# Optimization experiments

Hardware: AMD Instinct MI355X
Metric: run time of the kernel (lower is better)

The kernel has to match this reference:

```python
import jax, jax.numpy as jnp
import numpy as np

GROUP_SIZES = [5, 5, 5, 5, 5, 5, 4]  # 7 concept groups, sum = 34
LN_EPS = 1e-5


def setup_inputs() -> dict:
    key = jax.random.key(0)
    ks = jax.random.split(key, 12)
    B, N, D, K, P, C, NC, H = 256, 196, 768, 7, 512, 34, 7, 3072
    img_feat_map = jax.random.normal(ks[0], (B, N, D), dtype=jnp.float32)
    # torch: Embedding weight uniform in [-1/K, 1/K]
    vq_codebook = (jax.random.uniform(ks[1], (K, D), dtype=jnp.float32) * 2.0 - 1.0) / K
    agg_codebook = jax.random.normal(ks[2], (K, D), dtype=jnp.float32)
    W1 = jax.random.normal(ks[3], (D, H), dtype=jnp.float32) * 0.02
    b1 = jnp.zeros((H,), dtype=jnp.float32)
    W2 = jax.random.normal(ks[4], (H, D), dtype=jnp.float32) * 0.02
    b2 = jnp.zeros((D,), dtype=jnp.float32)
    ln_gamma = jnp.ones((D,), dtype=jnp.float32)
    ln_beta = jnp.zeros((D,), dtype=jnp.float32)
    W_proj = jax.random.normal(ks[5], (D, P), dtype=jnp.float32) * 0.02
    concept_emb = jax.random.normal(ks[6], (C, P), dtype=jnp.float32)
    concept_emb = concept_emb / jnp.linalg.norm(concept_emb, axis=-1, keepdims=True)
    cls_W = jax.random.normal(ks[7], (C, NC), dtype=jnp.float32) * 0.02
    cls_b = jnp.zeros((NC,), dtype=jnp.float32)
    logit_scale = jnp.float32(100.0)  # detached CLIP logit scale
    return {
        "img_feat_map": img_feat_map, "vq_codebook": vq_codebook,
        "agg_codebook": agg_codebook, "W1": W1, "b1": b1, "W2": W2, "b2": b2,
        "ln_gamma": ln_gamma, "ln_beta": ln_beta, "W_proj": W_proj,
        "concept_emb": concept_emb, "cls_W": cls_W, "cls_b": cls_b,
        "logit_scale": logit_scale,
    }


def _pairwise_sq_dists(x, cb):
    # x: [B, N, D], cb: [K, D] -> [B, N, K]
    x_sq = jnp.sum(x * x, axis=-1, keepdims=True)           # [B, N, 1]
    cb_sq = jnp.sum(cb * cb, axis=-1)                        # [K]
    dot = jnp.einsum("bnd,kd->bnk", x, cb)                  # [B, N, K]
    return x_sq + cb_sq - 2.0 * dot


def _avg_effective_rank(x, threshold=0.99):
    # x: [B, N, D]; per-sample SVD, rank = #{cumsum(S)/sum(S) <= thr}
    S = jnp.linalg.svd(jax.lax.stop_gradient(x), compute_uv=False)  # [B, min(N,D)]
    energy = jnp.cumsum(S, axis=-1) / jnp.sum(S, axis=-1, keepdims=True)
    ranks = jnp.sum(energy <= threshold, axis=-1)
    return jnp.mean(ranks.astype(jnp.float32))


def reference(img_feat_map, vq_codebook, agg_codebook, W1, b1, W2, b2,
              ln_gamma, ln_beta, W_proj, concept_emb, cls_W, cls_b, logit_scale):
    x = img_feat_map  # [B, N, D]

    avg_rank = _avg_effective_rank(x)

    # --- VectorQuantizeAggregator: soft assignment to 7 codes ---
    d_agg = _pairwise_sq_dists(x, agg_codebook)              # [B, N, K]
    soft = jax.nn.softmax(-d_agg, axis=-1)                   # [B, N, K]
    agg = jnp.einsum("bnk,bnd->bkd", soft, x)               # [B, K, D]

    # --- VectorQuantizer: hard argmin + gather (one-hot @ codebook) ---
    d_vq = _pairwise_sq_dists(x, vq_codebook)                # [B, N, K]
    idx = jnp.argmin(d_vq, axis=-1)                          # [B, N] int
    quantized = vq_codebook[idx]                             # [B, N, D] gather == onehot @ cb
    sg = jax.lax.stop_gradient
    codebook_loss = jnp.mean((quantized - sg(x)) ** 2)
    commitment_loss = jnp.mean((sg(quantized) - x) ** 2)
    vq_loss = codebook_loss + 1.0 * commitment_loss

    # --- bridge: FFN -> LayerNorm -> proj -> L2 normalize ---
    h = jax.nn.gelu(agg @ W1 + b1, approximate=False) @ W2 + b2  # [B, K, D]
    mu = jnp.mean(h, axis=-1, keepdims=True)
    var = jnp.mean((h - mu) ** 2, axis=-1, keepdims=True)
    hn = (h - mu) * jax.lax.rsqrt(var + LN_EPS) * ln_gamma + ln_beta
    tok = hn @ W_proj                                        # [B, K, 512]
    tok = tok / jnp.linalg.norm(tok, axis=-1, keepdims=True)

    # --- per-group concept logits: token g vs its concept slice ---
    logits_list = []
    start = 0
    for g, sz in enumerate(GROUP_SIZES):
        ce = concept_emb[start:start + sz]                   # [sz, 512]
        logits_list.append(logit_scale * (tok[:, g, :] @ ce.T))  # [B, sz]
        start += sz
    image_logits = jnp.concatenate(logits_list, axis=-1)     # [B, 34]

    cls_logits = image_logits @ cls_W + cls_b                # [B, 7]
    return (cls_logits, image_logits, vq_loss, avg_rank)
```

## Files before the change

kernel.cpp:

```cpp
#include <hip/hip_runtime.h>
#include <hip/hip_bf16.h>
#include <math.h>

using hbf = __hip_bfloat16;
typedef __bf16 bf16x8 __attribute__((ext_vector_type(8)));
typedef float f32x4 __attribute__((ext_vector_type(4)));

__device__ inline float r16d(float v){
  int x;
  x = __builtin_bit_cast(int, v);
  v += __builtin_bit_cast(float, __builtin_amdgcn_mov_dpp(x, 0x121, 0xf, 0xf, true));
  x = __builtin_bit_cast(int, v);
  v += __builtin_bit_cast(float, __builtin_amdgcn_mov_dpp(x, 0x122, 0xf, 0xf, true));
  x = __builtin_bit_cast(int, v);
  v += __builtin_bit_cast(float, __builtin_amdgcn_mov_dpp(x, 0x124, 0xf, 0xf, true));
  x = __builtin_bit_cast(int, v);
  v += __builtin_bit_cast(float, __builtin_amdgcn_mov_dpp(x, 0x128, 0xf, 0xf, true));
  return v;
}
__device__ inline void r16d4(float& a, float& b, float& c, float& d){
#define R16STAGE(ctl) { \
  int xa=__builtin_bit_cast(int,a), xb=__builtin_bit_cast(int,b); \
  int xc=__builtin_bit_cast(int,c), xd=__builtin_bit_cast(int,d); \
  a += __builtin_bit_cast(float, __builtin_amdgcn_mov_dpp(xa, ctl, 0xf, 0xf, true)); \
  b += __builtin_bit_cast(float, __builtin_amdgcn_mov_dpp(xb, ctl, 0xf, 0xf, true)); \
  c += __builtin_bit_cast(float, __builtin_amdgcn_mov_dpp(xc, ctl, 0xf, 0xf, true)); \
  d += __builtin_bit_cast(float, __builtin_amdgcn_mov_dpp(xd, ctl, 0xf, 0xf, true)); }
  R16STAGE(0x121) R16STAGE(0x122) R16STAGE(0x124) R16STAGE(0x128)
#undef R16STAGE
}
__device__ inline float wred(float v){
  v = r16d(v);
  v += __shfl_xor(v, 16);
  v += __shfl_xor(v, 32);
  return v;
}
__device__ inline float fast_rcp(float x){
  float r; asm("v_rcp_f32 %0, %1" : "=v"(r) : "v"(x)); return r;
}
__device__ inline float d4(const float4& a, const float4& b){
  return a.x*b.x + a.y*b.y + a.z*b.z + a.w*b.w;
}

__global__ void k_init(float* scal){
  if (threadIdx.x < 2) scal[threadIdx.x] = 0.f;
}

__global__ __launch_bounds__(512) void k_dist(const float* __restrict__ x,
    const float* __restrict__ vqcb, const float* __restrict__ agcb,
    hbf* __restrict__ aggbf, float* __restrict__ scal){
  __shared__ float cA[5376];
  __shared__ float cV[5376];
  __shared__ float sqA[7], sqV[7];
  const int tid = threadIdx.x, lane = tid & 63, wave = tid >> 6;
  const int b = blockIdx.x;
  for (int i = tid; i < 5376; i += 512){ cA[i] = agcb[i]; cV[i] = vqcb[i]; }
  __syncthreads();
  {
    int grp = tid >> 4, l16 = tid & 15;
    if (grp < 14){
      const float* s = (grp < 7) ? &cA[grp*768] : &cV[(grp-7)*768];
      float acc = 0.f;
      for (int j = l16; j < 768; j += 16) acc += s[j]*s[j];
      acc = r16d(acc);
      if (l16 == 0){ if (grp < 7) sqA[grp] = acc; else sqV[grp-7] = acc; }
    }
  }
  __syncthreads();
  float sqAr[7], sqVr[7];
#pragma unroll
  for (int k = 0; k < 7; ++k){ sqAr[k] = sqA[k]; sqVr[k] = sqV[k]; }

  float4 aR[7][3];
#pragma unroll
  for (int k = 0; k < 7; ++k)
#pragma unroll
    for (int c = 0; c < 3; ++c) aR[k][c] = make_float4(0.f,0.f,0.f,0.f);
  float loss = 0.f;

  const float* xb = x + (size_t)b*196*768;
  float4 cx0, cx1, cx2, nx0, nx1, nx2;
  { const float* p = xb + (size_t)wave*768 + (lane<<2);
    cx0 = *(const float4*)(p); cx1 = *(const float4*)(p+256); cx2 = *(const float4*)(p+512); }
  for (int it = 0; it < 25; ++it){
    const int n = it*8 + wave;
    const int nn = n + 8;
    if (nn < 196){
      const float* p = xb + (size_t)nn*768 + (lane<<2);
      nx0 = *(const float4*)(p); nx1 = *(const float4*)(p+256); nx2 = *(const float4*)(p+512);
    }
    if (n < 196){
      float xsq = d4(cx0,cx0)+d4(cx1,cx1)+d4(cx2,cx2);
      float dA[7], dV[7];
#pragma unroll
      for (int k = 0; k < 7; ++k){
        const float4* pa = (const float4*)&cA[k*768];
        const float4* pv = (const float4*)&cV[k*768];
        float4 a0 = pa[lane], a1 = pa[64+lane], a2 = pa[128+lane];
        float4 q0 = pv[lane], q1 = pv[64+lane], q2 = pv[128+lane];
        dA[k] = d4(cx0,a0)+d4(cx1,a1)+d4(cx2,a2);
        dV[k] = d4(cx0,q0)+d4(cx1,q1)+d4(cx2,q2);
      }
      xsq = wred(xsq);
#pragma unroll
      for (int k = 0; k < 7; ++k){ dA[k] = wred(dA[k]); dV[k] = wred(dV[k]); }
      float lg[7], mx = -1e30f;
#pragma unroll
      for (int k = 0; k < 7; ++k){ lg[k] = 2.f*dA[k] - sqAr[k]; mx = fmaxf(mx, lg[k]); }
      float pr[7], ssum = 0.f;
#pragma unroll
      for (int k = 0; k < 7; ++k){ pr[k] = expf(lg[k]-mx); ssum += pr[k]; }
      const float inv = 1.f/ssum;
      float mn = 1e30f;
#pragma unroll
      for (int k = 0; k < 7; ++k) mn = fminf(mn, sqVr[k] - 2.f*dV[k]);
      loss += xsq + mn;
#pragma unroll
      for (int k = 0; k < 7; ++k){
        const float w = pr[k]*inv;
        aR[k][0].x += w*cx0.x; aR[k][0].y += w*cx0.y; aR[k][0].z += w*cx0.z; aR[k][0].w += w*cx0.w;
        aR[k][1].x += w*cx1.x; aR[k][1].y += w*cx1.y; aR[k][1].z += w*cx1.z; aR[k][1].w += w*cx1.w;
        aR[k][2].x += w*cx2.x; aR[k][2].y += w*cx2.y; aR[k][2].z += w*cx2.z; aR[k][2].w += w*cx2.w;
      }
    }
    cx0 = nx0; cx1 = nx1; cx2 = nx2;
  }
  __syncthreads();
  for (int i = tid; i < 5376; i += 512) cA[i] = 0.f;
  __syncthreads();
  for (int w = 0; w < 8; ++w){
    if (wave == w){
#pragma unroll
      for (int k = 0; k < 7; ++k)
#pragma unroll
        for (int c = 0; c < 3; ++c){
          float* p = &cA[k*768 + c*256 + (lane<<2)];
          p[0] += aR[k][c].x; p[1] += aR[k][c].y; p[2] += aR[k][c].z; p[3] += aR[k][c].w;
        }
    }
    __syncthreads();
  }
  for (int i = tid; i < 5376; i += 512) aggbf[(size_t)b*5376 + i] = __float2bfloat16(cA[i]);
  if (lane == 0) atomicAdd(&scal[0], loss);
}

__global__ __launch_bounds__(512) void k_gram(const float* __restrict__ x, float* __restrict__ G){
  __shared__ hbf Xs[208*104];
  const int tid = threadIdx.x, lane = tid & 63, wave = tid >> 6;
  const int b = blockIdx.x;
  const int l15 = lane & 15;
  const int fr0 = wave, fr1 = wave + 8;
  const bool f1 = (fr1 < 13);
  f32x4 acc0[13] = {};
  f32x4 acc1[13] = {};
  const float* xb = x + (size_t)b*196*768;
  for (int kc = 0; kc < 8; ++kc){
    __syncthreads();
    for (int u = tid; u < 4992; u += 512){
      const int r = u / 24, c4 = u - r*24;
      ushort4 val;
      if (r < 196){
        float4 f = *(const float4*)(xb + (size_t)r*768 + kc*96 + c4*4);
        hbf t0 = __float2bfloat16(f.x), t1 = __float2bfloat16(f.y);
        hbf t2 = __float2bfloat16(f.z), t3 = __float2bfloat16(f.w);
        val.x = *(const unsigned short*)&t0; val.y = *(const unsigned short*)&t1;
        val.z = *(const unsigned short*)&t2; val.w = *(const unsigned short*)&t3;
      } else { val.x = 0; val.y = 0; val.z = 0; val.w = 0; }
      *(ushort4*)&Xs[r*104 + c4*4] = val;
    }
    __syncthreads();
#pragma unroll
    for (int kk = 0; kk < 3; ++kk){
      const int ko = kk*32 + (lane>>4)*8;
      bf16x8 a0 = *(const bf16x8*)&Xs[(fr0*16 + l15)*104 + ko];
      bf16x8 a1 = f1 ? *(const bf16x8*)&Xs[(fr1*16 + l15)*104 + ko] : a0;
#pragma unroll
      for (int fc = 0; fc < 13; ++fc){
        bf16x8 bb = *(const bf16x8*)&Xs[(fc*16 + l15)*104 + ko];
        acc0[fc] = __builtin_amdgcn_mfma_f32_16x16x32_bf16(a0, bb, acc0[fc], 0, 0, 0);
        if (f1) acc1[fc] = __builtin_amdgcn_mfma_f32_16x16x32_bf16(a1, bb, acc1[fc], 0, 0, 0);
      }
    }
  }
  const size_t gb = (size_t)b*38416;
  const int cr = (lane>>4)*4;
#pragma unroll
  for (int fc = 0; fc < 13; ++fc){
    const int gc = fc*16 + l15;
    if (gc < 196){
#pragma unroll
      for (int r = 0; r < 4; ++r){
        const int gr = fr0*16 + cr + r;
        if (gr < 196) G[gb + (size_t)gr*196 + gc] = acc0[fc][r];
      }
      if (f1){
#pragma unroll
        for (int r = 0; r < 4; ++r){
          const int gr = fr1*16 + cr + r;
          if (gr < 196) G[gb + (size_t)gr*196 + gc] = acc1[fc][r];
        }
      }
    }
  }
}

#define ESTR 200
#define FOLD4(vv4) { vv4.x = (oc==0)? v0 : vv4.x; vv4.y = (oc==1)? v0 : vv4.y; \
                     vv4.z = (oc==2)? v0 : vv4.z; vv4.w = (oc==3)? v0 : vv4.w; }
#define VHOIST(colc, out) { \
  const int col_ = (colc) + jc4; \
  const float4 xv_ = *(const float4*)(rowk + col_); \
  float4 vp_; \
  if (col_ > base){ vp_ = xv_; } \
  else if (col_ + 3 <= base){ vp_ = make_float4(0.f,0.f,0.f,0.f); } \
  else { vp_.x = 0.f; \
         vp_.y = (col_+1 > base) ? xv_.y : 0.f; \
         vp_.z = (col_+2 > base) ? xv_.z : 0.f; \
         vp_.w = xv_.w; } \
  out = vp_; sig += vp_.x*vp_.x + vp_.y*vp_.y + vp_.z*vp_.z + vp_.w*vp_.w; }

__global__ __launch_bounds__(1024) void k_eigen(const float* __restrict__ G, float* __restrict__ scal){
  extern __shared__ float S[];
  float* A   = S;
  float* ww  = S + 39200;
  float* dd  = S + 39456;
  float* ee  = S + 39656;
  float* e2  = S + 39856;
  float* red2= S + 40056;
  const int n = 196;
  const int tid = threadIdx.x, lane = tid & 63, wave = tid >> 6;
  const int grp = lane >> 4, c16 = lane & 15;
  const int jc4 = c16 << 2;
  const int rbase = (wave << 2) + grp;
  const int b = blockIdx.x;
  {
    const float4* Gv = (const float4*)(G + (size_t)b*38416);
    for (int u = tid; u < 9604; u += 1024){
      const int r = u / 49, c4 = u - r*49;
      *(float4*)(A + (size_t)r*ESTR + (c4<<2)) = Gv[u];
    }
    for (int r = tid; r < 196; r += 1024)
      *(float4*)(A + (size_t)r*ESTR + 196) = make_float4(0.f,0.f,0.f,0.f);
    if (tid < 256) ww[tid] = 0.f;
  }
  __syncthreads();
  for (int k = 0; k <= 130; ++k){
    const int base = k + 1, m = n - 1 - k;
    const float* rowk = &A[(size_t)k*ESTR];
    const float x0 = rowk[base];
    if (tid == 0) ww[k] = 0.f;
    float4 v4_0, v4_1, v4_2, v4_3;
    float sig = 0.f;
    VHOIST(0,   v4_0)
    VHOIST(64,  v4_1)
    VHOIST(128, v4_2)
    {
      const int col_ = 192 + jc4;
      const float4 xv_ = *(const float4*)(rowk + col_);
      if (c16 == 0){ v4_3 = xv_; sig += xv_.x*xv_.x + xv_.y*xv_.y + xv_.z*xv_.z + xv_.w*xv_.w; }
      else v4_3 = make_float4(0.f,0.f,0.f,0.f);
    }
    sig = r16d(sig);
    float tau = 0.f, v0 = 0.f, alpha = x0;
    if (sig > 1e-20f){
      const float mu = sqrtf(x0*x0 + sig);
      alpha = (x0 > 0.f) ? -mu : mu;
      v0 = x0 - alpha;
      tau = 2.f/(sig + v0*v0);
    }
    if (tid == 0) ee[k] = alpha;
    if (c16 == ((base >> 2) & 15)){
      const int oc = base & 3;
      const int op = base >> 6;
      if (op == 0){ FOLD4(v4_0) } else if (op == 1){ FOLD4(v4_1) } else { FOLD4(v4_2) }
    }
    const int p0 = base >> 6;
    const int i0 = rbase, i1 = 64 + rbase, i2 = 128 + rbase, i3 = 192 + rbase;
    float vr_0=0.f, vr_1=0.f, vr_2=0.f, vr_3=0.f;
    float wr_0=0.f, wr_1=0.f, wr_2=0.f, wr_3=0.f;
    if (tau != 0.f){
      float a0c=0.f, a1c=0.f, a2c=0.f, a3c=0.f;
      {
        const float* Ar = &A[(size_t)(base+i0)*ESTR];
        if (0 >= p0) a0c += d4(*(const float4*)(Ar + jc4),       v4_0);
        if (1 >= p0) a0c += d4(*(const float4*)(Ar + 64 + jc4),  v4_1);
        if (2 >= p0) a0c += d4(*(const float4*)(Ar + 128 + jc4), v4_2);
        a0c += d4(*(const float4*)(Ar + 192 + jc4), v4_3);
      }
      if (i1 < m){
        const float* Ar = &A[(size_t)(base+i1)*ESTR];
        if (0 >= p0) a1c += d4(*(const float4*)(Ar + jc4),       v4_0);
        if (1 >= p0) a1c += d4(*(const float4*)(Ar + 64 + jc4),  v4_1);
        if (2 >= p0) a1c += d4(*(const float4*)(Ar + 128 + jc4), v4_2);
        a1c += d4(*(const float4*)(Ar + 192 + jc4), v4_3);
      }
      if (i2 < m){
        const float* Ar = &A[(size_t)(base+i2)*ESTR];
        if (0 >= p0) a2c += d4(*(const float4*)(Ar + jc4),       v4_0);
        if (1 >= p0) a2c += d4(*(const float4*)(Ar + 64 + jc4),  v4_1);
        if (2 >= p0) a2c += d4(*(const float4*)(Ar + 128 + jc4), v4_2);
        a2c += d4(*(const float4*)(Ar + 192 + jc4), v4_3);
      }
      if (i3 < m){
        const float* Ar = &A[(size_t)(base+i3)*ESTR];
        if (0 >= p0) a3c += d4(*(const float4*)(Ar + jc4),       v4_0);
        if (1 >= p0) a3c += d4(*(const float4*)(Ar + 64 + jc4),  v4_1);
        if (2 >= p0) a3c += d4(*(const float4*)(Ar + 128 + jc4), v4_2);
        a3c += d4(*(const float4*)(Ar + 192 + jc4), v4_3);
      }
      r16d4(a0c, a1c, a2c, a3c);
      float cpart = 0.f;
      {
        wr_0 = tau*a0c;
        vr_0 = (i0 == 0) ? v0 : rowk[base+i0];
        cpart += vr_0*wr_0;
        if (c16 == 0) ww[base+i0] = wr_0;
      }
      if (i1 < m){
        wr_1 = tau*a1c; vr_1 = rowk[base+i1];
        cpart += vr_1*wr_1;
        if (c16 == 0) ww[base+i1] = wr_1;
      }
      if (i2 < m){
        wr_2 = tau*a2c; vr_2 = rowk[base+i2];
        cpart += vr_2*wr_2;
        if (c16 == 0) ww[base+i2] = wr_2;
      }
      if (i3 < m){
        wr_3 = tau*a3c; vr_3 = rowk[base+i3];
        cpart += vr_3*wr_3;
        if (c16 == 0) ww[base+i3] = wr_3;
      }
      cpart += __shfl_xor(cpart, 16);
      cpart += __shfl_xor(cpart, 32);
      if (lane == 0) red2[wave] = cpart;
    }
    __syncthreads();
    if (tau != 0.f){
      const float4* r2 = (const float4*)red2;
      const float4 q0 = r2[0], q1 = r2[1], q2 = r2[2], q3 = r2[3];
      const float vtw = (q0.x+q0.y+q0.z+q0.w) + (q1.x+q1.y+q1.z+q1.w)
                      + (q2.x+q2.y+q2.z+q2.w) + (q3.x+q3.y+q3.z+q3.w);
      const float c2 = 0.5f*tau*vtw;
      float4 w4_0, w4_1, w4_2, w4_3;
      { const float4 t4 = *(const float4*)(ww + jc4);
        w4_0.x = t4.x - c2*v4_0.x; w4_0.y = t4.y - c2*v4_0.y; w4_0.z = t4.z - c2*v4_0.z; w4_0.w = t4.w - c2*v4_0.w; }
      { const float4 t4 = *(const float4*)(ww + 64 + jc4);
        w4_1.x = t4.x - c2*v4_1.x; w4_1.y = t4.y - c2*v4_1.y; w4_1.z = t4.z - c2*v4_1.z; w4_1.w = t4.w - c2*v4_1.w; }
      { const float4 t4 = *(const float4*)(ww + 128 + jc4);
        w4_2.x = t4.x - c2*v4_2.x; w4_2.y = t4.y - c2*v4_2.y; w4_2.z = t4.z - c2*v4_2.z; w4_2.w = t4.w - c2*v4_2.w; }
      { const float4 t4 = *(const float4*)(ww + 192 + jc4);
        w4_3.x = t4.x - c2*v4_3.x; w4_3.y = t4.y - c2*v4_3.y; w4_3.z = t4.z - c2*v4_3.z; w4_3.w = t4.w - c2*v4_3.w; }
#define UP_T(IV, VRV, WRV) { \
      if (IV < m){ \
        const float vi = VRV; \
        const float wi = WRV - c2*vi; \
        float* Ar = &A[(size_t)(base+IV)*ESTR]; \
        if (0 >= p0){ float4 a = *(const float4*)(Ar + jc4); \
          a.x -= vi*w4_0.x + wi*v4_0.x; a.y -= vi*w4_0.y + wi*v4_0.y; \
          a.z -= vi*w4_0.z + wi*v4_0.z; a.w -= vi*w4_0.w + wi*v4_0.w; \
          *(float4*)(Ar + jc4) = a; } \
        if (1 >= p0){ float4 a = *(const float4*)(Ar + 64 + jc4); \
          a.x -= vi*w4_1.x + wi*v4_1.x; a.y -= vi*w4_1.y + wi*v4_1.y; \
          a.z -= vi*w4_1.z + wi*v4_1.z; a.w -= vi*w4_1.w + wi*v4_1.w; \
          *(float4*)(Ar + 64 + jc4) = a; } \
        if (2 >= p0){ float4 a = *(const float4*)(Ar + 128 + jc4); \
          a.x -= vi*w4_2.x + wi*v4_2.x; a.y -= vi*w4_2.y + wi*v4_2.y; \
          a.z -= vi*w4_2.z + wi*v4_2.z; a.w -= vi*w4_2.w + wi*v4_2.w; \
          *(float4*)(Ar + 128 + jc4) = a; } \
        if (c16 == 0){ float4 a = *(const float4*)(Ar + 192); \
          a.x -= vi*w4_3.x + wi*v4_3.x; a.y -= vi*w4_3.y + wi*v4_3.y; \
          a.z -= vi*w4_3.z + wi*v4_3.z; a.w -= vi*w4_3.w + wi*v4_3.w; \
          *(float4*)(Ar + 192) = a; } } }
      UP_T(i0, vr_0, wr_0)
      UP_T(i1, vr_1, wr_1)
      UP_T(i2, vr_2, wr_2)
      UP_T(i3, vr_3, wr_3)
#undef UP_T
    }
    __syncthreads();
  }
  if (wave == 0){
    float vrT[16], wrT[16];
    for (int k = 131; k <= n-3; ++k){
      const int base = k + 1, m = n - 1 - k;
      const float* rowk = &A[(size_t)k*ESTR];
      const float x0 = rowk[base];
      if (lane == 0) ww[k] = 0.f;
      float4 v4_2, v4_3;
      float sig = 0.f;
      VHOIST(128, v4_2)
      {
        const int col_ = 192 + jc4;
        float4 vp_ = make_float4(0.f,0.f,0.f,0.f);
        if (c16 == 0){
          const float4 xv_ = *(const float4*)(rowk + col_);
          if (col_ > base){ vp_ = xv_; }
          else { vp_.x = 0.f;
                 vp_.y = (col_+1 > base) ? xv_.y : 0.f;
                 vp_.z = (col_+2 > base) ? xv_.z : 0.f;
                 vp_.w = xv_.w; }
        }
        v4_3 = vp_; sig += vp_.x*vp_.x + vp_.y*vp_.y + vp_.z*vp_.z + vp_.w*vp_.w;
      }
      sig = r16d(sig);
      float tau = 0.f, v0 = 0.f, alpha = x0;
      if (sig > 1e-20f){
        const float mu = sqrtf(x0*x0 + sig);
        alpha = (x0 > 0.f) ? -mu : mu;
        v0 = x0 - alpha;
        tau = 2.f/(sig + v0*v0);
      }
      if (lane == 0) ee[k] = alpha;
      if (c16 == ((base >> 2) & 15)){
        const int oc = base & 3;
        if ((base >> 6) == 2){ FOLD4(v4_2) } else { FOLD4(v4_3) }
      }
      if (tau != 0.f){
        float cpart = 0.f;
#pragma unroll
        for (int t = 0; t < 16; ++t){
          const int i_ = (t << 2) + grp;
          float vrv = 0.f, wrv = 0.f;
          if (i_ < m){
            const float* Ar = &A[(size_t)(base+i_)*ESTR];
            const float4 a2 = *(const float4*)(Ar + 128 + jc4);
            const float4 a3 = *(const float4*)(Ar + 192 + jc4);
            float acc = d4(a2, v4_2) + d4(a3, v4_3);
            acc = r16d(acc);
            wrv = tau*acc;
            vrv = (i_ == 0) ? v0 : rowk[base+i_];
            cpart += vrv*wrv;
            if (c16 == 0) ww[base+i_] = wrv;
          }
          vrT[t] = vrv; wrT[t] = wrv;
        }
        cpart += __shfl_xor(cpart, 16);
        cpart += __shfl_xor(cpart, 32);
        const float c2 = 0.5f*tau*cpart;
        __threadfence_block();
        float4 w4_2, w4_3;
        { const float4 t4 = *(const float4*)(ww + 128 + jc4);
          w4_2.x = t4.x - c2*v4_2.x; w4_2.y = t4.y - c2*v4_2.y; w4_2.z = t4.z - c2*v4_2.z; w4_2.w = t4.w - c2*v4_2.w; }
        { const float4 t4 = *(const float4*)(ww + 192 + jc4);
          w4_3.x = t4.x - c2*v4_3.x; w4_3.y = t4.y - c2*v4_3.y; w4_3.z = t4.z - c2*v4_3.z; w4_3.w = t4.w - c2*v4_3.w; }
#pragma unroll
        for (int t = 0; t < 16; ++t){
          const int i_ = (t << 2) + grp;
          if (i_ < m){
            const float vi = vrT[t];
            const float wi = wrT[t] - c2*vi;
            float* Ar = &A[(size_t)(base+i_)*ESTR];
            float4 a = *(const float4*)(Ar + 128 + jc4);
            a.x -= vi*w4_2.x + wi*v4_2.x; a.y -= vi*w4_2.y + wi*v4_2.y;
            a.z -= vi*w4_2.z + wi*v4_2.z; a.w -= vi*w4_2.w + wi*v4_2.w;
            *(float4*)(Ar + 128 + jc4) = a;
            if (c16 == 0){
              float4 a3 = *(const float4*)(Ar + 192);
              a3.x -= vi*w4_3.x + wi*v4_3.x; a3.y -= vi*w4_3.y + wi*v4_3.y;
              a3.z -= vi*w4_3.z + wi*v4_3.z; a3.w -= vi*w4_3.w + wi*v4_3.w;
              *(float4*)(Ar + 192) = a3;
            }
          }
        }
        __threadfence_block();
      }
    }
  }
  __syncthreads();
  if (tid < n) dd[tid] = A[(size_t)tid*ESTR + tid];
  if (tid == 0) ee[n-2] = A[(size_t)(n-1)*ESTR + (n-2)];
  __syncthreads();
  if (tid < n-1) e2[tid] = ee[tid]*ee[tid];
  __syncthreads();
  float lo = 1e30f, hi = -1e30f;
  if (tid < n){
    const float rr = ((tid > 0) ? fabsf(ee[tid-1]) : 0.f) + ((tid < n-1) ? fabsf(ee[tid]) : 0.f);
    lo = dd[tid] - rr; hi = dd[tid] + rr;
  }
  {
    float l2 = lo, h2 = hi;
#pragma unroll
    for (int o = 32; o > 0; o >>= 1){
      l2 = fminf(l2, __shfl_xor(l2, o));
      h2 = fmaxf(h2, __shfl_xor(h2, o));
    }
    if (lane == 0){ ww[wave] = l2; red2[wave] = h2; }
  }
  __syncthreads();
  float glo = ww[0], ghi = red2[0];
#pragma unroll
  for (int w2 = 1; w2 < 16; ++w2){ glo = fminf(glo, ww[w2]); ghi = fmaxf(ghi, red2[w2]); }
  __syncthreads();
  float sv = 0.f;
  if (tid < n){
    float lob = glo, hib = ghi;
    for (int it2 = 0; it2 < 26; ++it2){
      const float mid = 0.5f*(lob + hib);
      float q = dd[0] - mid;
      int cnt = (q < 0.f) ? 1 : 0;
      for (int i = 1; i < n; ++i){
        const float r = fast_rcp(q);
        q = (dd[i] - mid) - e2[i-1]*r;
        q = (fabsf(q) < 1e-6f) ? -1e-6f : q;
        cnt += (q < 0.f) ? 1 : 0;
      }
      if (cnt <= tid) lob = mid; else hib = mid;
    }
    sv = sqrtf(fmaxf(0.5f*(lob + hib), 0.f));
  }
  __syncthreads();
  if (tid < n) ww[tid] = sv;
  __syncthreads();
  if (tid == 0){
    float tot = 0.f;
    for (int i = 0; i < n; ++i) tot += ww[i];
    const float thr = 0.99f*tot;
    float cs = 0.f; int rank = 0;
    for (int i = n-1; i >= 0; --i){ cs += ww[i]; rank += (cs <= thr) ? 1 : 0; }
    atomicAdd(&scal[1], (float)rank);
  }
}

__global__ __launch_bounds__(256) void k_tr(const float* __restrict__ in, hbf* __restrict__ outp,
                                            int Rr, int Cc){
  __shared__ float t[32][33];
  const int tid = threadIdx.x;
  const int lc = tid & 31, lr = tid >> 5;
  const int c0 = blockIdx.x*32, r0 = blockIdx.y*32;
#pragma unroll
  for (int i = 0; i < 4; ++i)
    t[lr + i*8][lc] = in[(size_t)(r0 + lr + i*8)*Cc + c0 + lc];
  __syncthreads();
#pragma unroll
  for (int i = 0; i < 4; ++i)
    outp[(size_t)(c0 + lr + i*8)*Rr + r0 + lc] = __float2bfloat16(t[lc][lr + i*8]);
}

template<int EPI>
__global__ __launch_bounds__(256) void k_gemm(const hbf* __restrict__ Aa, const hbf* __restrict__ Bb,
    const float* __restrict__ bias, void* __restrict__ outp, int Mi, int Ni, int Ki){
  __shared__ hbf As[64*72];
  __shared__ hbf Bs[64*72];
  const int tid = threadIdx.x, lane = tid & 63, wave = tid >> 6;
  const int row0 = blockIdx.y*64, col0 = blockIdx.x*64;
  const int m0 = (wave >> 1)*32, n0 = (wave & 1)*32;
  const int l15 = lane & 15, lk = (lane >> 4)*8;
  const int sr = tid >> 3, sc = (tid & 7)*8;
  f32x4 acc00 = {}, acc01 = {}, acc10 = {}, acc11 = {};
  for (int kt = 0; kt < Ki; kt += 64){
    __syncthreads();
    *(uint4*)&As[sr*72 + sc]        = *(const uint4*)&Aa[(size_t)(row0+sr)*Ki + kt + sc];
    *(uint4*)&As[(sr+32)*72 + sc]   = *(const uint4*)&Aa[(size_t)(row0+sr+32)*Ki + kt + sc];
    *(uint4*)&Bs[sr*72 + sc]        = *(const uint4*)&Bb[(size_t)(col0+sr)*Ki + kt + sc];
    *(uint4*)&Bs[(sr+32)*72 + sc]   = *(const uint4*)&Bb[(size_t)(col0+sr+32)*Ki + kt + sc];
    __syncthreads();
#pragma unroll
    for (int kk = 0; kk < 2; ++kk){
      const int ko = kk*32 + lk;
      bf16x8 a0 = *(const bf16x8*)&As[(m0 + l15)*72 + ko];
      bf16x8 a1 = *(const bf16x8*)&As[(m0 + 16 + l15)*72 + ko];
      bf16x8 b0 = *(const bf16x8*)&Bs[(n0 + l15)*72 + ko];
      bf16x8 b1 = *(const bf16x8*)&Bs[(n0 + 16 + l15)*72 + ko];
      acc00 = __builtin_amdgcn_mfma_f32_16x16x32_bf16(a0, b0, acc00, 0, 0, 0);
      acc01 = __builtin_amdgcn_mfma_f32_16x16x32_bf16(a0, b1, acc01, 0, 0, 0);
      acc10 = __builtin_amdgcn_mfma_f32_16x16x32_bf16(a1, b0, acc10, 0, 0, 0);
      acc11 = __builtin_amdgcn_mfma_f32_16x16x32_bf16(a1, b1, acc11, 0, 0, 0);
    }
  }
  const int cr = (lane >> 4)*4;
#pragma unroll
  for (int i = 0; i < 2; ++i){
#pragma unroll
    for (int j = 0; j < 2; ++j){
      f32x4 av = (i == 0) ? ((j == 0) ? acc00 : acc01) : ((j == 0) ? acc10 : acc11);
      const int gcol = col0 + n0 + j*16 + l15;
#pragma unroll
      for (int r = 0; r < 4; ++r){
        const int grow = row0 + m0 + i*16 + cr + r;
        float v = av[r];
        if (EPI == 1){
          v += bias[gcol];
          v = 0.5f*v*(1.f + erff(v*0.70710678118654752f));
          ((hbf*)outp)[(size_t)grow*Ni + gcol] = __float2bfloat16(v);
        } else if (EPI == 2){
          v += bias[gcol];
          ((float*)outp)[(size_t)grow*Ni + gcol] = v;
        } else {
          ((float*)outp)[(size_t)grow*Ni + gcol] = v;
        }
      }
    }
  }
}

__global__ __launch_bounds__(256) void k_ln(const float* __restrict__ h, const float* __restrict__ gam,
    const float* __restrict__ bet, hbf* __restrict__ hn){
  const int tid = threadIdx.x, lane = tid & 63, wave = tid >> 6;
  const int row = blockIdx.x*4 + wave;
  const float* hr = h + (size_t)row*768;
  const int off = lane*4;
  float4 v0 = *(const float4*)(hr + off);
  float4 v1 = *(const float4*)(hr + 256 + off);
  float4 v2 = *(const float4*)(hr + 512 + off);
  float s = v0.x+v0.y+v0.z+v0.w + v1.x+v1.y+v1.z+v1.w + v2.x+v2.y+v2.z+v2.w;
  s = wred(s);
  const float mu = s*(1.f/768.f);
  float q = 0.f;
  q += (v0.x-mu)*(v0.x-mu); q += (v0.y-mu)*(v0.y-mu); q += (v0.z-mu)*(v0.z-mu); q += (v0.w-mu)*(v0.w-mu);
  q += (v1.x-mu)*(v1.x-mu); q += (v1.y-mu)*(v1.y-mu); q += (v1.z-mu)*(v1.z-mu); q += (v1.w-mu)*(v1.w-mu);
  q += (v2.x-mu)*(v2.x-mu); q += (v2.y-mu)*(v2.y-mu); q += (v2.z-mu)*(v2.z-mu); q += (v2.w-mu)*(v2.w-mu);
  q = wred(q);
  const float rs = 1.f/sqrtf(q*(1.f/768.f) + 1e-5f);
  float4 g0 = *(const float4*)(gam + off), g1 = *(const float4*)(gam + 256 + off), g2 = *(const float4*)(gam + 512 + off);
  float4 t0 = *(const float4*)(bet + off), t1 = *(const float4*)(bet + 256 + off), t2 = *(const float4*)(bet + 512 + off);
  hbf* o = hn + (size_t)row*768;
  o[off+0] = __float2bfloat16((v0.x-mu)*rs*g0.x + t0.x);
  o[off+1] = __float2bfloat16((v0.y-mu)*rs*g0.y + t0.y);
  o[off+2] = __float2bfloat16((v0.z-mu)*rs*g0.z + t0.z);
  o[off+3] = __float2bfloat16((v0.w-mu)*rs*g0.w + t0.w);
  o[256+off+0] = __float2bfloat16((v1.x-mu)*rs*g1.x + t1.x);
  o[256+off+1] = __float2bfloat16((v1.y-mu)*rs*g1.y + t1.y);
  o[256+off+2] = __float2bfloat16((v1.z-mu)*rs*g1.z + t1.z);
  o[256+off+3] = __float2bfloat16((v1.w-mu)*rs*g1.w + t1.w);
  o[512+off+0] = __float2bfloat16((v2.x-mu)*rs*g2.x + t2.x);
  o[512+off+1] = __float2bfloat16((v2.y-mu)*rs*g2.y + t2.y);
  o[512+off+2] = __float2bfloat16((v2.z-mu)*rs*g2.z + t2.z);
  o[512+off+3] = __float2bfloat16((v2.w-mu)*rs*g2.w + t2.w);
}

__global__ __launch_bounds__(256) void k_head(const float* __restrict__ tok, const float* __restrict__ ce,
    const float* __restrict__ clsW, const float* __restrict__ clsb, const float* __restrict__ lgs,
    float* __restrict__ out){
  __shared__ float tkn[7*512];
  __shared__ float il[40];
  const int tid = threadIdx.x, lane = tid & 63, wave = tid >> 6;
  const int b = blockIdx.x;
  const float ls = lgs[0];
  for (int g = wave; g < 7; g += 4){
    const float* tr = tok + (size_t)(b*7 + g)*512;
    float4 u0 = *(const float4*)(tr + (lane<<3));
    float4 u1 = *(const float4*)(tr + (lane<<3) + 4);
    float s = d4(u0,u0) + d4(u1,u1);
    s = wred(s);
    const float inv = 1.f/sqrtf(s);
    float* dst = &tkn[g*512 + (lane<<3)];
    dst[0] = u0.x*inv; dst[1] = u0.y*inv; dst[2] = u0.z*inv; dst[3] = u0.w*inv;
    dst[4] = u1.x*inv; dst[5] = u1.y*inv; dst[6] = u1.z*inv; dst[7] = u1.w*inv;
  }
  __syncthreads();
  for (int c = wave; c < 34; c += 4){
    const int g = (c < 30) ? (c/5) : 6;
    const float* tp = &tkn[g*512 + (lane<<3)];
    const float* cp = ce + (size_t)c*512 + (lane<<3);
    float s = tp[0]*cp[0] + tp[1]*cp[1] + tp[2]*cp[2] + tp[3]*cp[3]
            + tp[4]*cp[4] + tp[5]*cp[5] + tp[6]*cp[6] + tp[7]*cp[7];
    s = wred(s);
    if (lane == 0){
      const float v = ls*s;
      il[c] = v;
      out[1792 + b*34 + c] = v;
    }
  }
  __syncthreads();
  if (tid < 7){
    float s = clsb[tid];
    for (int c = 0; c < 34; ++c) s += il[c]*clsW[c*7 + tid];
    out[b*7 + tid] = s;
  }
}

__global__ void k_fin(const float* __restrict__ scal, float* __restrict__ out){
  if (threadIdx.x == 0){
    out[10496] = 2.f*scal[0]/(float)(256*196*768);
    out[10497] = scal[1]*(1.f/256.f);
  }
}

extern "C" void kernel_launch(void* const* d_in, const int* in_sizes, int n_in,
                              void* d_out, int out_size, void* d_ws, size_t ws_size,
                              hipStream_t stream) {
  (void)in_sizes; (void)n_in; (void)out_size; (void)ws_size;
  const float* x    = (const float*)d_in[0];
  const float* vqcb = (const float*)d_in[1];
  const float* agcb = (const float*)d_in[2];
  const float* W1   = (const float*)d_in[3];
  const float* b1   = (const float*)d_in[4];
  const float* W2   = (const float*)d_in[5];
  const float* b2   = (const float*)d_in[6];
  const float* gam  = (const float*)d_in[7];
  const float* bet  = (const float*)d_in[8];
  const float* Wp   = (const float*)d_in[9];
  const float* ce   = (const float*)d_in[10];
  const float* clsW = (const float*)d_in[11];
  const float* clsb = (const float*)d_in[12];
  const float* lgs  = (const float*)d_in[13];
  float* out = (float*)d_out;
  char* w = (char*)d_ws;

  float* scal  = (float*)w;
  float* G     = (float*)(w + 256);
  hbf*   aggbf = (hbf*)(w + 39338240ULL);
  hbf*   W1t   = (hbf*)(w + 42090752ULL);
  hbf*   W2t   = (hbf*)(w + 46809344ULL);
  hbf*   Wpt   = (hbf*)(w + 51527936ULL);
  hbf*   h1    = (hbf*)(w + 256);
  float* hbuf  = (float*)(w + 256 + 16777216ULL);
  hbf*   hn    = (hbf*)(w + 256 + 25165824ULL);
  float* tok   = (float*)(w + 256 + 29360128ULL);

  k_init<<<dim3(1), dim3(64), 0, stream>>>(scal);
  k_dist<<<dim3(256), dim3(512), 0, stream>>>(x, vqcb, agcb, aggbf, scal);
  k_gram<<<dim3(256), dim3(512), 0, stream>>>(x, G);
  const int EIG_SMEM = 40072*4;
  hipFuncSetAttribute((const void*)k_eigen, hipFuncAttributeMaxDynamicSharedMemorySize, EIG_SMEM);
  k_eigen<<<dim3(256), dim3(1024), EIG_SMEM, stream>>>(G, scal);
  k_tr<<<dim3(96,24), dim3(256), 0, stream>>>(W1, W1t, 768, 3072);
  k_tr<<<dim3(24,96), dim3(256), 0, stream>>>(W2, W2t, 3072, 768);
  k_tr<<<dim3(16,24), dim3(256), 0, stream>>>(Wp, Wpt, 768, 512);
  k_gemm<1><<<dim3(48,28), dim3(256), 0, stream>>>(aggbf, W1t, b1, (void*)h1, 1792, 3072, 768);
  k_gemm<2><<<dim3(12,28), dim3(256), 0, stream>>>(h1, W2t, b2, (void*)hbuf, 1792, 768, 3072);
  k_ln<<<dim3(448), dim3(256), 0, stream>>>(hbuf, gam, bet, hn);
  k_gemm<3><<<dim3(8,28), dim3(256), 0, stream>>>(hn, Wpt, nullptr, (void*)tok, 1792, 512, 768);
  k_head<<<dim3(256), dim3(256), 0, stream>>>(tok, ce, clsW, clsb, lgs, out);
  k_fin<<<dim3(1), dim3(64), 0, stream>>>(scal, out);
}
```

Baseline: 1.069 ms.

## Compact eigen smem stride, reuse matvec loads in rank-2 update, trim bisection

New measurement: 1.072 ms. No clear change (+0.2%).

```diff
diff --git a/kernel.cpp b/kernel.cpp
--- a/kernel.cpp
+++ b/kernel.cpp
@@ -204,7 +204,7 @@
   }
 }
 
-#define ESTR 200
+#define ESTR 196
 #define FOLD4(vv4) { vv4.x = (oc==0)? v0 : vv4.x; vv4.y = (oc==1)? v0 : vv4.y; \
                      vv4.z = (oc==2)? v0 : vv4.z; vv4.w = (oc==3)? v0 : vv4.w; }
 #define VHOIST(colc, out) { \
@@ -222,11 +222,11 @@
 __global__ __launch_bounds__(1024) void k_eigen(const float* __restrict__ G, float* __restrict__ scal){
   extern __shared__ float S[];
   float* A   = S;
-  float* ww  = S + 39200;
-  float* dd  = S + 39456;
-  float* ee  = S + 39656;
-  float* e2  = S + 39856;
-  float* red2= S + 40056;
+  float* ww  = S + 38496;
+  float* dd  = S + 38752;
+  float* ee  = S + 38952;
+  float* e2  = S + 39152;
+  float* red2= S + 39352;
   const int n = 196;
   const int tid = threadIdx.x, lane = tid & 63, wave = tid >> 6;
   const int grp = lane >> 4, c16 = lane & 15;
@@ -235,12 +235,9 @@
   const int b = blockIdx.x;
   {
     const float4* Gv = (const float4*)(G + (size_t)b*38416);
-    for (int u = tid; u < 9604; u += 1024){
-      const int r = u / 49, c4 = u - r*49;
-      *(float4*)(A + (size_t)r*ESTR + (c4<<2)) = Gv[u];
-    }
-    for (int r = tid; r < 196; r += 1024)
-      *(float4*)(A + (size_t)r*ESTR + 196) = make_float4(0.f,0.f,0.f,0.f);
+    float4* Av = (float4*)A;
+    for (int u = tid; u < 9604; u += 1024) Av[u] = Gv[u];
+    if (tid < 80) S[38416 + tid] = 0.f;
     if (tid < 256) ww[tid] = 0.f;
   }
   __syncthreads();
@@ -255,10 +252,12 @@
     VHOIST(64,  v4_1)
     VHOIST(128, v4_2)
     {
-      const int col_ = 192 + jc4;
-      const float4 xv_ = *(const float4*)(rowk + col_);
-      if (c16 == 0){ v4_3 = xv_; sig += xv_.x*xv_.x + xv_.y*xv_.y + xv_.z*xv_.z + xv_.w*xv_.w; }
-      else v4_3 = make_float4(0.f,0.f,0.f,0.f);
+      float4 vp_ = make_float4(0.f,0.f,0.f,0.f);
+      if (c16 == 0){
+        vp_ = *(const float4*)(rowk + 192);
+        sig += vp_.x*vp_.x + vp_.y*vp_.y + vp_.z*vp_.z + vp_.w*vp_.w;
+      }
+      v4_3 = vp_;
     }
     sig = r16d(sig);
     float tau = 0.f, v0 = 0.f, alpha = x0;
@@ -278,36 +277,24 @@
     const int i0 = rbase, i1 = 64 + rbase, i2 = 128 + rbase, i3 = 192 + rbase;
     float vr_0=0.f, vr_1=0.f, vr_2=0.f, vr_3=0.f;
     float wr_0=0.f, wr_1=0.f, wr_2=0.f, wr_3=0.f;
+    float4 cA0={}, cA1={}, cA2={};
+    float4 cB0={}, cB1={}, cB2={};
+    float4 cC0={}, cC1={}, cC2={};
+    float4 cD0={}, cD1={}, cD2={};
     if (tau != 0.f){
       float a0c=0.f, a1c=0.f, a2c=0.f, a3c=0.f;
-      {
-        const float* Ar = &A[(size_t)(base+i0)*ESTR];
-        if (0 >= p0) a0c += d4(*(const float4*)(Ar + jc4),       v4_0);
-        if (1 >= p0) a0c += d4(*(const float4*)(Ar + 64 + jc4),  v4_1);
-        if (2 >= p0) a0c += d4(*(const float4*)(Ar + 128 + jc4), v4_2);
-        a0c += d4(*(const float4*)(Ar + 192 + jc4), v4_3);
-      }
-      if (i1 < m){
-        const float* Ar = &A[(size_t)(base+i1)*ESTR];
-        if (0 >= p0) a1c += d4(*(const float4*)(Ar + jc4),       v4_0);
-        if (1 >= p0) a1c += d4(*(const float4*)(Ar + 64 + jc4),  v4_1);
-        if (2 >= p0) a1c += d4(*(const float4*)(Ar + 128 + jc4), v4_2);
-        a1c += d4(*(const float4*)(Ar + 192 + jc4), v4_3);
-      }
-      if (i2 < m){
-        const float* Ar = &A[(size_t)(base+i2)*ESTR];
-        if (0 >= p0) a2c += d4(*(const float4*)(Ar + jc4),       v4_0);
-        if (1 >= p0) a2c += d4(*(const float4*)(Ar + 64 + jc4),  v4_1);
-        if (2 >= p0) a2c += d4(*(const float4*)(Ar + 128 + jc4), v4_2);
-        a2c += d4(*(const float4*)(Ar + 192 + jc4), v4_3);
-      }
-      if (i3 < m){
-        const float* Ar = &A[(size_t)(base+i3)*ESTR];
-        if (0 >= p0) a3c += d4(*(const float4*)(Ar + jc4),       v4_0);
-        if (1 >= p0) a3c += d4(*(const float4*)(Ar + 64 + jc4),  v4_1);
-        if (2 >= p0) a3c += d4(*(const float4*)(Ar + 128 + jc4), v4_2);
-        a3c += d4(*(const float4*)(Ar + 192 + jc4), v4_3);
-      }
+#define MV_T(IV, ACC, R0, R1, R2) { \
+      if (IV < m){ \
+        const float* Ar = &A[(size_t)(base+IV)*ESTR]; \
+        if (0 >= p0){ R0 = *(const float4*)(Ar + jc4);       ACC += d4(R0, v4_0); } \
+        if (1 >= p0){ R1 = *(const float4*)(Ar + 64 + jc4);  ACC += d4(R1, v4_1); } \
+        if (2 >= p0){ R2 = *(const float4*)(Ar + 128 + jc4); ACC += d4(R2, v4_2); } \
+        if (c16 == 0){ ACC += d4(*(const float4*)(Ar + 192), v4_3); } } }
+      MV_T(i0, a0c, cA0, cA1, cA2)
+      MV_T(i1, a1c, cB0, cB1, cB2)
+      MV_T(i2, a2c, cC0, cC1, cC2)
+      MV_T(i3, a3c, cD0, cD1, cD2)
+#undef MV_T
       r16d4(a0c, a1c, a2c, a3c);
       float cpart = 0.f;
       {
@@ -342,40 +329,41 @@
       const float vtw = (q0.x+q0.y+q0.z+q0.w) + (q1.x+q1.y+q1.z+q1.w)
                       + (q2.x+q2.y+q2.z+q2.w) + (q3.x+q3.y+q3.z+q3.w);
       const float c2 = 0.5f*tau*vtw;
-      float4 w4_0, w4_1, w4_2, w4_3;
+      float4 w4_0, w4_1, w4_2, w4_3 = make_float4(0.f,0.f,0.f,0.f);
       { const float4 t4 = *(const float4*)(ww + jc4);
         w4_0.x = t4.x - c2*v4_0.x; w4_0.y = t4.y - c2*v4_0.y; w4_0.z = t4.z - c2*v4_0.z; w4_0.w = t4.w - c2*v4_0.w; }
       { const float4 t4 = *(const float4*)(ww + 64 + jc4);
         w4_1.x = t4.x - c2*v4_1.x; w4_1.y = t4.y - c2*v4_1.y; w4_1.z = t4.z - c2*v4_1.z; w4_1.w = t4.w - c2*v4_1.w; }
       { const float4 t4 = *(const float4*)(ww + 128 + jc4);
         w4_2.x = t4.x - c2*v4_2.x; w4_2.y = t4.y - c2*v4_2.y; w4_2.z = t4.z - c2*v4_2.z; w4_2.w = t4.w - c2*v4_2.w; }
-      { const float4 t4 = *(const float4*)(ww + 192 + jc4);
+      if (c16 == 0){
+        const float4 t4 = *(const float4*)(ww + 192);
         w4_3.x = t4.x - c2*v4_3.x; w4_3.y = t4.y - c2*v4_3.y; w4_3.z = t4.z - c2*v4_3.z; w4_3.w = t4.w - c2*v4_3.w; }
-#define UP_T(IV, VRV, WRV) { \
+#define UP_T(IV, VRV, WRV, R0, R1, R2) { \
       if (IV < m){ \
         const float vi = VRV; \
         const float wi = WRV - c2*vi; \
         float* Ar = &A[(size_t)(base+IV)*ESTR]; \
-        if (0 >= p0){ float4 a = *(const float4*)(Ar + jc4); \
-          a.x -= vi*w4_0.x + wi*v4_0.x; a.y -= vi*w4_0.y + wi*v4_0.y; \
-          a.z -= vi*w4_0.z + wi*v4_0.z; a.w -= vi*w4_0.w + wi*v4_0.w; \
-          *(float4*)(Ar + jc4) = a; } \
-        if (1 >= p0){ float4 a = *(const float4*)(Ar + 64 + jc4); \
-          a.x -= vi*w4_1.x + wi*v4_1.x; a.y -= vi*w4_1.y + wi*v4_1.y; \
-          a.z -= vi*w4_1.z + wi*v4_1.z; a.w -= vi*w4_1.w + wi*v4_1.w; \
-          *(float4*)(Ar + 64 + jc4) = a; } \
-        if (2 >= p0){ float4 a = *(const float4*)(Ar + 128 + jc4); \
-          a.x -= vi*w4_2.x + wi*v4_2.x; a.y -= vi*w4_2.y + wi*v4_2.y; \
-          a.z -= vi*w4_2.z + wi*v4_2.z; a.w -= vi*w4_2.w + wi*v4_2.w; \
-          *(float4*)(Ar + 128 + jc4) = a; } \
+        if (0 >= p0){ \
+          R0.x -= vi*w4_0.x + wi*v4_0.x; R0.y -= vi*w4_0.y + wi*v4_0.y; \
+          R0.z -= vi*w4_0.z + wi*v4_0.z; R0.w -= vi*w4_0.w + wi*v4_0.w; \
+          *(float4*)(Ar + jc4) = R0; } \
+        if (1 >= p0){ \
+          R1.x -= vi*w4_1.x + wi*v4_1.x; R1.y -= vi*w4_1.y + wi*v4_1.y; \
+          R1.z -= vi*w4_1.z + wi*v4_1.z; R1.w -= vi*w4_1.w + wi*v4_1.w; \
+          *(float4*)(Ar + 64 + jc4) = R1; } \
+        if (2 >= p0){ \
+          R2.x -= vi*w4_2.x + wi*v4_2.x; R2.y -= vi*w4_2.y + wi*v4_2.y; \
+          R2.z -= vi*w4_2.z + wi*v4_2.z; R2.w -= vi*w4_2.w + wi*v4_2.w; \
+          *(float4*)(Ar + 128 + jc4) = R2; } \
         if (c16 == 0){ float4 a = *(const float4*)(Ar + 192); \
           a.x -= vi*w4_3.x + wi*v4_3.x; a.y -= vi*w4_3.y + wi*v4_3.y; \
           a.z -= vi*w4_3.z + wi*v4_3.z; a.w -= vi*w4_3.w + wi*v4_3.w; \
           *(float4*)(Ar + 192) = a; } } }
-      UP_T(i0, vr_0, wr_0)
-      UP_T(i1, vr_1, wr_1)
-      UP_T(i2, vr_2, wr_2)
-      UP_T(i3, vr_3, wr_3)
+      UP_T(i0, vr_0, wr_0, cA0, cA1, cA2)
+      UP_T(i1, vr_1, wr_1, cB0, cB1, cB2)
+      UP_T(i2, vr_2, wr_2, cC0, cC1, cC2)
+      UP_T(i3, vr_3, wr_3, cD0, cD1, cD2)
 #undef UP_T
     }
     __syncthreads();
@@ -391,14 +379,13 @@
       float sig = 0.f;
       VHOIST(128, v4_2)
       {
-        const int col_ = 192 + jc4;
         float4 vp_ = make_float4(0.f,0.f,0.f,0.f);
         if (c16 == 0){
-          const float4 xv_ = *(const float4*)(rowk + col_);
-          if (col_ > base){ vp_ = xv_; }
+          const float4 xv_ = *(const float4*)(rowk + 192);
+          if (192 > base){ vp_ = xv_; }
           else { vp_.x = 0.f;
-                 vp_.y = (col_+1 > base) ? xv_.y : 0.f;
-                 vp_.z = (col_+2 > base) ? xv_.z : 0.f;
+                 vp_.y = (193 > base) ? xv_.y : 0.f;
+                 vp_.z = (194 > base) ? xv_.z : 0.f;
                  vp_.w = xv_.w; }
         }
         v4_3 = vp_; sig += vp_.x*vp_.x + vp_.y*vp_.y + vp_.z*vp_.z + vp_.w*vp_.w;
@@ -424,9 +411,8 @@
           float vrv = 0.f, wrv = 0.f;
           if (i_ < m){
             const float* Ar = &A[(size_t)(base+i_)*ESTR];
-            const float4 a2 = *(const float4*)(Ar + 128 + jc4);
-            const float4 a3 = *(const float4*)(Ar + 192 + jc4);
-            float acc = d4(a2, v4_2) + d4(a3, v4_3);
+            float acc = d4(*(const float4*)(Ar + 128 + jc4), v4_2);
+            if (c16 == 0) acc += d4(*(const float4*)(Ar + 192), v4_3);
             acc = r16d(acc);
             wrv = tau*acc;
             vrv = (i_ == 0) ? v0 : rowk[base+i_];
@@ -439,10 +425,11 @@
         cpart += __shfl_xor(cpart, 32);
         const float c2 = 0.5f*tau*cpart;
         __threadfence_block();
-        float4 w4_2, w4_3;
+        float4 w4_2, w4_3 = make_float4(0.f,0.f,0.f,0.f);
         { const float4 t4 = *(const float4*)(ww + 128 + jc4);
           w4_2.x = t4.x - c2*v4_2.x; w4_2.y = t4.y - c2*v4_2.y; w4_2.z = t4.z - c2*v4_2.z; w4_2.w = t4.w - c2*v4_2.w; }
-        { const float4 t4 = *(const float4*)(ww + 192 + jc4);
+        if (c16 == 0){
+          const float4 t4 = *(const float4*)(ww + 192);
           w4_3.x = t4.x - c2*v4_3.x; w4_3.y = t4.y - c2*v4_3.y; w4_3.z = t4.z - c2*v4_3.z; w4_3.w = t4.w - c2*v4_3.w; }
 #pragma unroll
         for (int t = 0; t < 16; ++t){
@@ -495,7 +482,7 @@
   float sv = 0.f;
   if (tid < n){
     float lob = glo, hib = ghi;
-    for (int it2 = 0; it2 < 26; ++it2){
+    for (int it2 = 0; it2 < 18; ++it2){
       const float mid = 0.5f*(lob + hib);
       float q = dd[0] - mid;
       int cnt = (q < 0.f) ? 1 : 0;
@@ -712,7 +699,7 @@
   k_init<<<dim3(1), dim3(64), 0, stream>>>(scal);
   k_dist<<<dim3(256), dim3(512), 0, stream>>>(x, vqcb, agcb, aggbf, scal);
   k_gram<<<dim3(256), dim3(512), 0, stream>>>(x, G);
-  const int EIG_SMEM = 40072*4;
+  const int EIG_SMEM = 39368*4;
   hipFuncSetAttribute((const void*)k_eigen, hipFuncAttributeMaxDynamicSharedMemorySize, EIG_SMEM);
   k_eigen<<<dim3(256), dim3(1024), EIG_SMEM, stream>>>(G, scal);
   k_tr<<<dim3(96,24), dim3(256), 0, stream>>>(W1, W1t, 768, 3072);
```
